# Performance work log

Hardware: AMD Instinct MI355X
Metric: run time of the kernel (lower is better)

The kernel has to match this reference:

```python
import jax, jax.numpy as jnp
import numpy as np

N_NODES = 100000
N_EDGES = 1600000
NUM_FEATURES = 48
HIDDEN = 256
NUM_CLASSES = 1


def setup_inputs() -> dict:
    key = jax.random.key(0)
    k1, k2, k3, k4 = jax.random.split(key, 4)
    x = jax.random.normal(k1, (N_NODES, NUM_FEATURES), dtype=jnp.float32)
    edge_index = jax.random.randint(k2, (2, N_EDGES), 0, N_NODES, dtype=jnp.int32)
    W1 = jax.random.normal(k3, (NUM_FEATURES, HIDDEN), dtype=jnp.float32) / np.sqrt(NUM_FEATURES)
    W2 = jax.random.normal(k4, (HIDDEN, NUM_CLASSES), dtype=jnp.float32) / np.sqrt(HIDDEN)
    bias = jnp.zeros((NUM_CLASSES,), dtype=jnp.float32)
    b2 = jnp.zeros((NUM_CLASSES,), dtype=jnp.float32)
    return {"x": x, "edge_index": edge_index, "W1": W1, "bias": bias, "W2": W2, "b2": b2}


def _gcn_propagate(x, edge_index, num_nodes):
    # Add self-loops.
    loop = jnp.arange(num_nodes, dtype=edge_index.dtype)
    row = jnp.concatenate([edge_index[0], loop])  # source nodes
    col = jnp.concatenate([edge_index[1], loop])  # destination nodes
    # Symmetric normalization D^{-1/2} A D^{-1/2}.
    ones = jnp.ones(col.shape[0], dtype=x.dtype)
    deg = jax.ops.segment_sum(ones, col, num_segments=num_nodes)
    dinv = jax.lax.rsqrt(jnp.maximum(deg, 1.0))
    norm = dinv[row] * dinv[col]  # [E+N]
    # Gather-scale-scatter: memory-bound edge aggregation.
    msg = x[row] * norm[:, None]  # [E+N, F]
    return jax.ops.segment_sum(msg, col, num_segments=num_nodes)  # [N, F]


def reference(x, edge_index, W1, bias, W2, b2):
    h = _gcn_propagate(x, edge_index, x.shape[0])  # [N, F]
    h = h @ W1 + bias                               # [N, H] (+ broadcast bias, C==1)
    h = h @ W2 + b2                                 # [N, C]
    return h
```

## Files before the change

### kernel.cpp

```cpp
#include <hip/hip_runtime.h>


constexpr int kNodes  = 100000;
constexpr int kEdges  = 1600000;
constexpr int kFeat   = 48;
constexpr int kHidden = 256;

constexpr int kBShift = 9;
constexpr int kBSize  = 1 << kBShift;
constexpr int kNB     = (kNodes + kBSize - 1) / kBSize;
constexpr int kCap    = 10240;
constexpr int kEPB    = 8192;
constexpr int kQuads  = kEdges / 4;
constexpr int kBBlk   = (kEdges + kEPB - 1) / kEPB;
constexpr int kZBlk   = (kNodes + 255) / 256;

__global__ __launch_bounds__(256) void fat_kernel(const int* __restrict__ row,
                                                  const int* __restrict__ col,
                                                  const float* __restrict__ x,
                                                  const float* __restrict__ W1,
                                                  const float* __restrict__ W2,
                                                  int* __restrict__ cursor,
                                                  int* __restrict__ bpacked,
                                                  float* __restrict__ z) {
    if (blockIdx.x < kBBlk) {
        __shared__ int hist[kNB];
        int tid = threadIdx.x;
        for (int t = tid; t < kNB; t += 256) hist[t] = 0;
        __syncthreads();

        int qbase = blockIdx.x * (kEPB / 4);
        const int4* colq = reinterpret_cast<const int4*>(col);
        const int4* rowq = reinterpret_cast<const int4*>(row);
        int4 c4[8];
        #pragma unroll
        for (int k = 0; k < 8; ++k) {
            int q = qbase + k * 256 + tid;
            if (q < kQuads) {
                int4 c = colq[q];
                c4[k] = c;
                atomicAdd(&hist[c.x >> kBShift], 1);
                atomicAdd(&hist[c.y >> kBShift], 1);
                atomicAdd(&hist[c.z >> kBShift], 1);
                atomicAdd(&hist[c.w >> kBShift], 1);
            } else {
                c4[k] = make_int4(-1, -1, -1, -1);
            }
        }
        __syncthreads();
        for (int t = tid; t < kNB; t += 256) {
            int c = hist[t];
            hist[t] = c ? atomicAdd(&cursor[t], c) : 0;
        }
        __syncthreads();
        #pragma unroll
        for (int k = 0; k < 8; ++k) {
            int q = qbase + k * 256 + tid;
            if (q < kQuads) {
                int4 r = rowq[q];
                int cs[4] = {c4[k].x, c4[k].y, c4[k].z, c4[k].w};
                int rs[4] = {r.x, r.y, r.z, r.w};
                #pragma unroll
                for (int u = 0; u < 4; ++u) {
                    int c = cs[u], b = c >> kBShift;
                    int slot = atomicAdd(&hist[b], 1);
                    if (slot < kCap)
                        bpacked[b * kCap + slot] = ((c & (kBSize - 1)) << 17) | rs[u];
                }
            }
        }
    } else {
        __shared__ float sw2[kHidden];
        __shared__ float spart[kFeat * 4];
        __shared__ float sw[kFeat];
        int tid = threadIdx.x;
        sw2[tid] = W2[tid];
        __syncthreads();
        if (tid < kFeat * 4) {
            int t = tid >> 2, q = tid & 3;
            const float4* wr = reinterpret_cast<const float4*>(W1 + t * kHidden + q * 64);
            const float4* b4 = reinterpret_cast<const float4*>(sw2) + q * 16;
            float a = 0.f;
            #pragma unroll
            for (int j = 0; j < 16; ++j) {
                float4 u = wr[j];
                float4 v = b4[j];
                a += u.x * v.x + u.y * v.y + u.z * v.z + u.w * v.w;
            }
            spart[tid] = a;
        }
        __syncthreads();
        if (tid < kFeat)
            sw[tid] = spart[4 * tid] + spart[4 * tid + 1]
                    + spart[4 * tid + 2] + spart[4 * tid + 3];
        __syncthreads();
        int i = (blockIdx.x - kBBlk) * 256 + tid;
        if (i < kNodes) {
            const float4* xp = reinterpret_cast<const float4*>(x + (size_t)i * kFeat);
            float acc = 0.f;
            #pragma unroll
            for (int k = 0; k < kFeat / 4; ++k) {
                float4 v = xp[k];
                acc += v.x * sw[4 * k + 0] + v.y * sw[4 * k + 1]
                     + v.z * sw[4 * k + 2] + v.w * sw[4 * k + 3];
            }
            z[i] = acc;
        }
    }
}

__global__ __launch_bounds__(1024) void degfin_kernel(const int* __restrict__ cursor,
                                                      const int* __restrict__ bpacked,
                                                      const float* __restrict__ z,
                                                      float* __restrict__ dinv,
                                                      float* __restrict__ dy) {
    __shared__ int sdeg[kBSize];
    int b = blockIdx.x, tid = threadIdx.x;
    if (tid < kBSize) sdeg[tid] = 0;
    __syncthreads();
    int n = min(cursor[b], kCap);
    int base = b * kCap;
    const int4* bq = reinterpret_cast<const int4*>(bpacked + base);
    int nq = n >> 2;
    for (int i = tid; i < nq; i += 1024) {
        int4 p = bq[i];
        atomicAdd(&sdeg[p.x >> 17], 1);
        atomicAdd(&sdeg[p.y >> 17], 1);
        atomicAdd(&sdeg[p.z >> 17], 1);
        atomicAdd(&sdeg[p.w >> 17], 1);
    }
    if (tid < (n & 3)) atomicAdd(&sdeg[bpacked[base + (n & ~3) + tid] >> 17], 1);
    __syncthreads();
    int node = b * kBSize + tid;
    if (tid < kBSize && node < kNodes) {
        float d  = (float)(sdeg[tid] + 1);
        float di = rsqrtf(d);
        dinv[node] = di;
        dy[node]   = di * z[node];
    }
}

__global__ __launch_bounds__(1024) void agg_kernel(const int* __restrict__ cursor,
                                                   const int* __restrict__ bpacked,
                                                   const float* __restrict__ dy,
                                                   const float* __restrict__ dinv,
                                                   const float* __restrict__ bias,
                                                   const float* __restrict__ W2,
                                                   const float* __restrict__ b2,
                                                   float* __restrict__ out) {
    __shared__ float ssum[kBSize];
    __shared__ float sc;
    int b = blockIdx.x, tid = threadIdx.x;
    if (tid < kBSize) ssum[tid] = 0.f;
    if (tid < 64) {
        const float4* w2q = reinterpret_cast<const float4*>(W2);
        float4 v = w2q[tid];
        float s = v.x + v.y + v.z + v.w;
        #pragma unroll
        for (int o = 32; o > 0; o >>= 1) s += __shfl_down(s, o);
        if (tid == 0) sc = bias[0] * s + b2[0];
    }
    __syncthreads();
    int n = min(cursor[b], kCap);
    int base = b * kCap;
    const int4* bq = reinterpret_cast<const int4*>(bpacked + base);
    int nq = n >> 2;
    for (int i = tid; i < nq; i += 1024) {
        int4 p = bq[i];
        atomicAdd(&ssum[p.x >> 17], dy[p.x & 0x1FFFF]);
        atomicAdd(&ssum[p.y >> 17], dy[p.y & 0x1FFFF]);
        atomicAdd(&ssum[p.z >> 17], dy[p.z & 0x1FFFF]);
        atomicAdd(&ssum[p.w >> 17], dy[p.w & 0x1FFFF]);
    }
    if (tid < (n & 3)) {
        int p = bpacked[base + (n & ~3) + tid];
        atomicAdd(&ssum[p >> 17], dy[p & 0x1FFFF]);
    }
    __syncthreads();
    int node = b * kBSize + tid;
    if (tid < kBSize && node < kNodes)
        out[node] = dinv[node] * (ssum[tid] + dy[node]) + sc;
}

extern "C" void kernel_launch(void* const* d_in, const int* in_sizes, int n_in,
                              void* d_out, int out_size, void* d_ws, size_t ws_size,
                              hipStream_t stream) {
    const float* x    = (const float*)d_in[0];
    const int*   ei   = (const int*)d_in[1];
    const float* W1   = (const float*)d_in[2];
    const float* bias = (const float*)d_in[3];
    const float* W2   = (const float*)d_in[4];
    const float* b2   = (const float*)d_in[5];
    float*       out  = (float*)d_out;

    const int* row = ei;
    const int* col = ei + kEdges;

    char*  p       = (char*)d_ws;
    int*   cursor  = (int*)p;                   p += 1024;
    float* z       = (float*)p;                 p += (size_t)kNodes * 4;
    float* dinv    = (float*)p;                 p += (size_t)kNodes * 4;
    float* dy      = (float*)p;                 p += (size_t)kNodes * 4;
    int*   bpacked = (int*)p;

    hipMemsetAsync(cursor, 0, kNB * sizeof(int), stream);
    fat_kernel<<<kBBlk + kZBlk, 256, 0, stream>>>(row, col, x, W1, W2, cursor, bpacked, z);
    degfin_kernel<<<kNB, 1024, 0, stream>>>(cursor, bpacked, z, dinv, dy);
    agg_kernel<<<kNB, 1024, 0, stream>>>(cursor, bpacked, dy, dinv, bias, W2, b2, out);
}
```

Baseline: 111.9 us.

## Stage bucketed edges in shared memory and write contiguous runs per bucket

The bucketing pass now computes a local prefix scan of per-bucket counts, scatters packed edges into a shared-memory staging buffer, and then has each wave copy a bucket's contiguous run to global memory. This replaces the scattered per-edge global stores with coalesced writes. The block size doubles to 512 threads with half the unrolled loads per thread, and the z-computation blocks reuse the staging buffer. The cost is extra barriers for the scan and 32KB+ of LDS per block, which may reduce occupancy.

```diff
diff --git a/kernel.cpp b/kernel.cpp
--- a/kernel.cpp
+++ b/kernel.cpp
@@ -8,14 +8,14 @@
 
 constexpr int kBShift = 9;
 constexpr int kBSize  = 1 << kBShift;
-constexpr int kNB     = (kNodes + kBSize - 1) / kBSize;
-constexpr int kCap    = 10240;
+constexpr int kNB     = 196;
 constexpr int kEPB    = 8192;
 constexpr int kQuads  = kEdges / 4;
 constexpr int kBBlk   = (kEdges + kEPB - 1) / kEPB;
-constexpr int kZBlk   = (kNodes + 255) / 256;
-
-__global__ __launch_bounds__(256) void fat_kernel(const int* __restrict__ row,
+constexpr int kZBlk   = (kNodes + 511) / 512;
+constexpr int kCap    = 10240;
+
+__global__ __launch_bounds__(512) void fat_kernel(const int* __restrict__ row,
                                                   const int* __restrict__ col,
                                                   const float* __restrict__ x,
                                                   const float* __restrict__ W1,
@@ -23,39 +23,56 @@
                                                   int* __restrict__ cursor,
                                                   int* __restrict__ bpacked,
                                                   float* __restrict__ z) {
+    __shared__ int stage[kEPB];
+    __shared__ int hist[256];
+    __shared__ int lstart[256];
+    __shared__ int lcur[256];
+    __shared__ int gbase[256];
+    __shared__ int scan[256];
+    const int tid = threadIdx.x;
+
     if (blockIdx.x < kBBlk) {
-        __shared__ int hist[kNB];
-        int tid = threadIdx.x;
-        for (int t = tid; t < kNB; t += 256) hist[t] = 0;
+        if (tid < 256) hist[tid] = 0;
         __syncthreads();
 
         int qbase = blockIdx.x * (kEPB / 4);
         const int4* colq = reinterpret_cast<const int4*>(col);
         const int4* rowq = reinterpret_cast<const int4*>(row);
-        int4 c4[8];
+        int4 c4[4];
         #pragma unroll
-        for (int k = 0; k < 8; ++k) {
-            int q = qbase + k * 256 + tid;
+        for (int k = 0; k < 4; ++k) {
+            int q = qbase + k * 512 + tid;
             if (q < kQuads) {
-                int4 c = colq[q];
-                c4[k] = c;
-                atomicAdd(&hist[c.x >> kBShift], 1);
-                atomicAdd(&hist[c.y >> kBShift], 1);
-                atomicAdd(&hist[c.z >> kBShift], 1);
-                atomicAdd(&hist[c.w >> kBShift], 1);
+                c4[k] = colq[q];
+                atomicAdd(&hist[c4[k].x >> kBShift], 1);
+                atomicAdd(&hist[c4[k].y >> kBShift], 1);
+                atomicAdd(&hist[c4[k].z >> kBShift], 1);
+                atomicAdd(&hist[c4[k].w >> kBShift], 1);
             } else {
                 c4[k] = make_int4(-1, -1, -1, -1);
             }
         }
         __syncthreads();
-        for (int t = tid; t < kNB; t += 256) {
-            int c = hist[t];
-            hist[t] = c ? atomicAdd(&cursor[t], c) : 0;
+        int h = 0;
+        if (tid < 256) { h = hist[tid]; scan[tid] = h; }
+        __syncthreads();
+        for (int off = 1; off < 256; off <<= 1) {
+            int v = 0;
+            if (tid < 256 && tid >= off) v = scan[tid - off];
+            __syncthreads();
+            if (tid < 256) scan[tid] += v;
+            __syncthreads();
+        }
+        if (tid < 256) {
+            int ls = scan[tid] - h;
+            lstart[tid] = ls;
+            lcur[tid]   = ls;
+            gbase[tid]  = (tid < kNB && h > 0) ? atomicAdd(&cursor[tid], h) : 0;
         }
         __syncthreads();
         #pragma unroll
-        for (int k = 0; k < 8; ++k) {
-            int q = qbase + k * 256 + tid;
+        for (int k = 0; k < 4; ++k) {
+            int q = qbase + k * 512 + tid;
             if (q < kQuads) {
                 int4 r = rowq[q];
                 int cs[4] = {c4[k].x, c4[k].y, c4[k].z, c4[k].w};
@@ -63,18 +80,27 @@
                 #pragma unroll
                 for (int u = 0; u < 4; ++u) {
                     int c = cs[u], b = c >> kBShift;
-                    int slot = atomicAdd(&hist[b], 1);
-                    if (slot < kCap)
-                        bpacked[b * kCap + slot] = ((c & (kBSize - 1)) << 17) | rs[u];
+                    int s = atomicAdd(&lcur[b], 1);
+                    stage[s] = ((c & (kBSize - 1)) << 17) | rs[u];
                 }
             }
         }
+        __syncthreads();
+        int wave = tid >> 6, lane = tid & 63;
+        for (int b = wave; b < kNB; b += 8) {
+            int n  = hist[b];
+            int ls = lstart[b];
+            int gb = gbase[b];
+            for (int i = lane; i < n; i += 64) {
+                int g = gb + i;
+                if (g < kCap) bpacked[b * kCap + g] = stage[ls + i];
+            }
+        }
     } else {
-        __shared__ float sw2[kHidden];
-        __shared__ float spart[kFeat * 4];
-        __shared__ float sw[kFeat];
-        int tid = threadIdx.x;
-        sw2[tid] = W2[tid];
+        float* sw2   = reinterpret_cast<float*>(stage);
+        float* spart = reinterpret_cast<float*>(stage) + 256;
+        float* swv   = reinterpret_cast<float*>(stage) + 512;
+        if (tid < kHidden) sw2[tid] = W2[tid];
         __syncthreads();
         if (tid < kFeat * 4) {
             int t = tid >> 2, q = tid & 3;
@@ -91,18 +117,18 @@
         }
         __syncthreads();
         if (tid < kFeat)
-            sw[tid] = spart[4 * tid] + spart[4 * tid + 1]
-                    + spart[4 * tid + 2] + spart[4 * tid + 3];
-        __syncthreads();
-        int i = (blockIdx.x - kBBlk) * 256 + tid;
+            swv[tid] = spart[4 * tid] + spart[4 * tid + 1]
+                     + spart[4 * tid + 2] + spart[4 * tid + 3];
+        __syncthreads();
+        int i = (blockIdx.x - kBBlk) * 512 + tid;
         if (i < kNodes) {
             const float4* xp = reinterpret_cast<const float4*>(x + (size_t)i * kFeat);
             float acc = 0.f;
             #pragma unroll
             for (int k = 0; k < kFeat / 4; ++k) {
                 float4 v = xp[k];
-                acc += v.x * sw[4 * k + 0] + v.y * sw[4 * k + 1]
-                     + v.z * sw[4 * k + 2] + v.w * sw[4 * k + 3];
+                acc += v.x * swv[4 * k + 0] + v.y * swv[4 * k + 1]
+                     + v.z * swv[4 * k + 2] + v.w * swv[4 * k + 3];
             }
             z[i] = acc;
         }
@@ -204,7 +230,7 @@
     int*   bpacked = (int*)p;
 
     hipMemsetAsync(cursor, 0, kNB * sizeof(int), stream);
-    fat_kernel<<<kBBlk + kZBlk, 256, 0, stream>>>(row, col, x, W1, W2, cursor, bpacked, z);
+    fat_kernel<<<kBBlk + kZBlk, 512, 0, stream>>>(row, col, x, W1, W2, cursor, bpacked, z);
     degfin_kernel<<<kNB, 1024, 0, stream>>>(cursor, bpacked, z, dinv, dy);
     agg_kernel<<<kNB, 1024, 0, stream>>>(cursor, bpacked, dy, dinv, bias, W2, b2, out);
 }
```

New measurement: 108.4 us. 3.1% less time.
